# Kernel optimization log

Hardware: AMD Instinct MI355X
Metric: run time of the kernel (lower is better)

Reference implementation:

```python
import jax, jax.numpy as jnp
import numpy as np

N = 16384
C = 4        # in_channels
K = 16       # neighbors
H = 64       # mlp width


def setup_inputs() -> dict:
    key = jax.random.key(0)
    k0, k1, k2, k3, k4 = jax.random.split(key, 5)
    x = jax.random.normal(k0, (N, C), dtype=jnp.float32)
    # nn.Linear(2C, 64) and nn.Linear(64, 64): weight [out, in], bias [out]
    W1 = jax.random.normal(k1, (H, 2 * C), dtype=jnp.float32) * (1.0 / np.sqrt(2 * C))
    b1 = jax.random.normal(k2, (H,), dtype=jnp.float32) * 0.01
    W2 = jax.random.normal(k3, (H, H), dtype=jnp.float32) * (1.0 / np.sqrt(H))
    b2 = jax.random.normal(k4, (H,), dtype=jnp.float32) * 0.01
    return {"x": x, "W1": W1, "b1": b1, "W2": W2, "b2": b2}


def reference(x, W1, b1, W2, b2):
    # x: [N, C] single point cloud (torch code unsqueezes batch dim 0)
    xs = jax.lax.stop_gradient(x)  # knn indices computed under no_grad
    # pairwise = -||xi - xj||^2 = 2*xi.xj - ||xi||^2 - ||xj||^2
    xx = jnp.sum(xs * xs, axis=1)                      # [N]
    pairwise = 2.0 * (xs @ xs.T) - xx[:, None] - xx[None, :]  # [N, N]
    _, idx = jax.lax.top_k(pairwise, K)                # [N, K] (self included, dist 0 is max)
    neigh = x[idx]                                     # [N, K, C] gather
    center = jnp.broadcast_to(x[:, None, :], (x.shape[0], K, C))
    edge = jnp.concatenate([neigh - center, center], axis=-1)  # [N, K, 2C]
    h = jax.nn.relu(jnp.einsum('nkc,hc->nkh', edge, W1) + b1)
    h = jax.nn.relu(jnp.einsum('nkh,gh->nkg', h, W2) + b2)     # [N, K, H]
    out = jnp.mean(h, axis=1)                          # [N, H]
    return out[None]                                   # [1, N, H] matches torch output
```

## Files before the change

### kernel.cpp

```cpp
#include <hip/hip_runtime.h>
#include <math.h>

#define N_PTS 16384
#define K_NBR 16
#define H_DIM 64
#define CAP   38
#define NBLK  (N_PTS / 16)
#define HBLK  (NBLK / 2)
#define PBLK  (HBLK / 4)

typedef unsigned long long u64;
typedef unsigned short u16;
typedef float v2f   __attribute__((ext_vector_type(2)));
typedef float f32x4 __attribute__((ext_vector_type(4)));
typedef short bf16x8 __attribute__((ext_vector_type(8)));

__device__ __forceinline__ u64 mkkey(unsigned vbits, unsigned idx) {
    unsigned of = vbits ^ (unsigned)(((int)vbits >> 31) | 0x80000000);
    return ((u64)of << 32) | (unsigned)(~idx);
}
__device__ __forceinline__ unsigned keyidx(u64 k) { return ~(unsigned)k; }

__device__ __forceinline__ float readlane_f(float v, int l) {
    return __uint_as_float(__builtin_amdgcn_readlane(__float_as_uint(v), l));
}

__device__ __forceinline__ unsigned ofsbits(float f) {
    unsigned b = __float_as_uint(f);
    return b ^ ((unsigned)((int)b >> 31) | 0x80000000u);
}
__device__ __forceinline__ float inv_ofs(unsigned u) {
    return __uint_as_float(u ^ (~(unsigned)((int)u >> 31) | 0x80000000u));
}

__device__ __forceinline__ u16 f2bf(float f) {
    unsigned u = __float_as_uint(f);
    return (u16)((u + 0x7FFFu + ((u >> 16) & 1u)) >> 16);
}
__device__ __forceinline__ float bf2f(u16 b) {
    return __uint_as_float(((unsigned)b) << 16);
}

__device__ __forceinline__ float wave_sort_f32(float v, int lane) {
#pragma unroll
    for (int k = 2; k <= 64; k <<= 1) {
#pragma unroll
        for (int j = k >> 1; j > 0; j >>= 1) {
            float o = __shfl_xor(v, j, 64);
            bool keep_min = (((lane & k) == 0) == ((lane & j) == 0));
            v = keep_min ? fminf(v, o) : fmaxf(v, o);
        }
    }
    return v;
}
__device__ __forceinline__ u64 wave_sort_u64(u64 v, int lane) {
#pragma unroll
    for (int k = 2; k <= 64; k <<= 1) {
#pragma unroll
        for (int j = k >> 1; j > 0; j >>= 1) {
            u64 o = __shfl_xor((unsigned long long)v, j, 64);
            bool keep_min = (((lane & k) == 0) == ((lane & j) == 0));
            u64 mn = (v < o) ? v : o;
            u64 mx = (v < o) ? o : v;
            v = keep_min ? mn : mx;
        }
    }
    return v;
}
__device__ __forceinline__ u64 half32_sort_u64(u64 v, int lane) {
    const int l = lane & 31;
#pragma unroll
    for (int k = 2; k <= 32; k <<= 1) {
#pragma unroll
        for (int j = k >> 1; j > 0; j >>= 1) {
            u64 o = __shfl_xor((unsigned long long)v, j, 64);
            bool keep_min = (((l & k) == 0) == ((l & j) == 0));
            u64 mn = (v < o) ? v : o;
            u64 mx = (v < o) ? o : v;
            v = keep_min ? mn : mx;
        }
    }
    return v;
}

struct CompRes { int nc; float tau; };
__device__ __attribute__((noinline)) CompRes wave_compact(uint2* buf, int cnt,
                                                          int lane) {
    float lm = -INFINITY;
    for (int s = lane; s < cnt; s += 64)
        lm = fmaxf(lm, __uint_as_float(buf[s].x));
    const float tv = readlane_f(wave_sort_f32(lm, lane), 48);
    int nc = 0;
    for (int s0 = 0; s0 < cnt; s0 += 64) {
        const int s = s0 + lane;
        uint2 e = make_uint2(0u, 0u);
        bool keep = false;
        if (s < cnt) { e = buf[s]; keep = (__uint_as_float(e.x) >= tv); }
        const u64 km = __ballot(keep);
        if (keep) {
            int pfx = (int)__popcll(km & ((1ull << lane) - 1));
            buf[nc + pfx] = e;
        }
        nc += (int)__popcll(km);
    }
    CompRes r; r.nc = nc; r.tau = tv;
    return r;
}

__global__ __launch_bounds__(256) void prep_kernel(const float4* __restrict__ x4,
                                                   u16* __restrict__ bf) {
    const int i = blockIdx.x * 256 + threadIdx.x;
    const float4 v = x4[i];
    float xx;
    {
#pragma clang fp contract(off)
        float s0 = v.x * v.x, s1 = v.y * v.y, s2 = v.z * v.z, s3 = v.w * v.w;
        xx = ((s0 + s1) + s2) + s3;
    }
    float c[4] = {v.x, v.y, v.z, v.w};
    u16 H[4], M[4], L[4];
#pragma unroll
    for (int q = 0; q < 4; ++q) {
        float f = c[q];
        u16 h = f2bf(f);            float fh = bf2f(h);
        u16 m = f2bf(f - fh);       float fm = bf2f(m);
        u16 l = f2bf(f - fh - fm);
        H[q] = h; M[q] = m; L[q] = l;
    }
    const float nx = -xx;
    u16 X0 = f2bf(nx);              float x0f = bf2f(X0);
    u16 X1 = f2bf(nx - x0f);        float x1f = bf2f(X1);
    u16 X2 = f2bf(nx - x0f - x1f);
    u16 o[32];
#pragma unroll
    for (int q = 0; q < 4; ++q) {
        o[q]      = H[q];
        o[4 + q]  = M[q];
        o[8 + q]  = H[q];
        o[12 + q] = L[q];
        o[16 + q] = H[q];
        o[20 + q] = M[q];
    }
    o[24] = X0; o[25] = X1; o[26] = X2;
    o[27] = 0; o[28] = 0; o[29] = 0; o[30] = 0; o[31] = 0;
    uint4* dst = (uint4*)(bf + (size_t)i * 32);
#pragma unroll
    for (int q2 = 0; q2 < 4; ++q2) {
        uint4 w;
        w.x = (unsigned)o[q2 * 8 + 0] | ((unsigned)o[q2 * 8 + 1] << 16);
        w.y = (unsigned)o[q2 * 8 + 2] | ((unsigned)o[q2 * 8 + 3] << 16);
        w.z = (unsigned)o[q2 * 8 + 4] | ((unsigned)o[q2 * 8 + 5] << 16);
        w.w = (unsigned)o[q2 * 8 + 6] | ((unsigned)o[q2 * 8 + 7] << 16);
        dst[q2] = w;
    }
}

__global__ __launch_bounds__(256, 4) void knn_kernel(
        const float4* __restrict__ x4,
        const u16* __restrict__ bfrag,
        unsigned* __restrict__ vals,
        u16* __restrict__ idxs) {
    __shared__ __align__(16) uint2 buf[4][16][CAP];
    __shared__ unsigned tau_sh[16];
    const int lane = threadIdx.x & 63;
    const int wave = threadIdx.x >> 6;
    const int q    = lane & 15;
    const int g    = lane >> 4;
    const int qgrp = blockIdx.x >> 1;
    const int half = blockIdx.x & 1;
    const int rowbase = qgrp * 16;
    const int pblk = half * HBLK + wave * PBLK;

    const float4 xi = x4[rowbase + q];
    u16 Ha[4], Ma[4], La[4];
    {
        float yy[4] = {2.f * xi.x, 2.f * xi.y, 2.f * xi.z, 2.f * xi.w};
#pragma unroll
        for (int c = 0; c < 4; ++c) {
            u16 h = f2bf(yy[c]);             float fh = bf2f(h);
            u16 m = f2bf(yy[c] - fh);        float fm = bf2f(m);
            u16 l = f2bf(yy[c] - fh - fm);
            Ha[c] = h; Ma[c] = m; La[c] = l;
        }
    }
    bf16x8 qfrag;
    {
        const u16 ONEB = 0x3F80;
#pragma unroll
        for (int c = 0; c < 4; ++c) {
            u16 lo, hi;
            if (g == 0)      { lo = Ha[c]; hi = Ha[c]; }
            else if (g == 1) { lo = Ma[c]; hi = Ha[c]; }
            else if (g == 2) { lo = La[c]; hi = Ma[c]; }
            else             { lo = (c < 3) ? ONEB : 0; hi = 0; }
            qfrag[c]     = (short)lo;
            qfrag[c + 4] = (short)hi;
        }
    }
    const f32x4 zacc = {0.f, 0.f, 0.f, 0.f};
    const bf16x8* bp = (const bf16x8*)bfrag + (size_t)pblk * 64 + (q * 4 + g);

    f32x4 mx = {-INFINITY, -INFINITY, -INFINITY, -INFINITY};
    {
        bf16x8 A0[4], A1[4];
#pragma unroll
        for (int i = 0; i < 4; ++i) A0[i] = bp[(2 * i) * 64];
#pragma unroll
        for (int i = 0; i < 4; ++i) A1[i] = bp[(8 + 2 * i) * 64];
        const bf16x8* pa = bp + 16 * 64;

#define PROCA(BUF) do {                                                      \
    _Pragma("unroll")                                                        \
    for (int i = 0; i < 4; ++i) {                                            \
        const f32x4 aa = __builtin_amdgcn_mfma_f32_16x16x32_bf16(            \
            BUF[i], qfrag, zacc, 0, 0, 0);                                   \
        mx[0] = fmaxf(mx[0], aa[0]); mx[1] = fmaxf(mx[1], aa[1]);            \
        mx[2] = fmaxf(mx[2], aa[2]); mx[3] = fmaxf(mx[3], aa[3]);            \
    }                                                                        \
} while (0)

        for (int it = 0; it < 7; ++it) {
            PROCA(A0);
#pragma unroll
            for (int i = 0; i < 4; ++i) A0[i] = pa[(2 * i) * 64];
            PROCA(A1);
#pragma unroll
            for (int i = 0; i < 4; ++i) A1[i] = pa[(8 + 2 * i) * 64];
            pa += 16 * 64;
        }
        PROCA(A0);
        PROCA(A1);
#undef PROCA
    }

    {
        float* am = (float*)&buf[0][0][0];
        const int base = wave * 256 + q * 16 + g * 4;
        am[base + 0] = mx[0]; am[base + 1] = mx[1];
        am[base + 2] = mx[2]; am[base + 3] = mx[3];
        __syncthreads();
#pragma unroll
        for (int rr = 0; rr < 4; ++rr) {
            const int r = wave * 4 + rr;
            float v = am[(lane >> 4) * 256 + r * 16 + (lane & 15)];
            v = wave_sort_f32(v, lane);
            if (lane == 48) tau_sh[r] = ofsbits(v);
        }
        __syncthreads();
    }
    float tau = inv_ofs(tau_sh[q]);

    unsigned cq = 0;
    uint2* bq = &buf[wave][q][0];
    const unsigned gid4 = (unsigned)(g * 4);

#define INSERT4(AV, CB) do {                                                 \
    for (;;) {                                                               \
        const bool k0 = (AV)[0] >= tau, k1 = (AV)[1] >= tau;                 \
        const bool k2 = (AV)[2] >= tau, k3 = (AV)[3] >= tau;                 \
        const int cnt = (int)k0 + (int)k1 + (int)k2 + (int)k3;               \
        const int sa = __shfl_xor(cnt, 16, 64);                              \
        const int sb = __shfl_xor(cnt, 32, 64);                              \
        const int sc = __shfl_xor(sa, 32, 64);                               \
        const int tot = cnt + sa + sb + sc;                                  \
        const int pf  = ((g & 1) ? sa : 0) + ((g & 2) ? (sb + sc) : 0);      \
        const u64 ovm = __ballot(cq + (unsigned)tot > CAP);                  \
        if (__builtin_expect(ovm == 0, 1)) {                                 \
            unsigned slot = cq + (unsigned)pf;                               \
            if (k0) bq[slot++] = make_uint2(__float_as_uint((AV)[0]), (CB)); \
            if (k1) bq[slot++] = make_uint2(__float_as_uint((AV)[1]), (CB)+1);\
            if (k2) bq[slot++] = make_uint2(__float_as_uint((AV)[2]), (CB)+2);\
            if (k3) bq[slot++] = make_uint2(__float_as_uint((AV)[3]), (CB)+3);\
            cq += (unsigned)tot;                                             \
            break;                                                           \
        }                                                                    \
        u64 ov = ovm & 0xFFFFull;                                            \
        while (ov) {                                                         \
            const int r = (int)__builtin_ctzll(ov); ov &= ov - 1;            \
            const unsigned cr =                                              \
                (unsigned)__builtin_amdgcn_readlane((int)cq, r);             \
            CompRes res = wave_compact(&buf[wave][r][0], (int)cr, lane);     \
            if (q == r) { cq = (unsigned)res.nc;                             \
                          tau = fmaxf(tau, res.tau); }                       \
        }                                                                    \
    }                                                                        \
} while (0)

#define PROC4(BUF, TB) do {                                                  \
    f32x4 A4_[4];                                                            \
    _Pragma("unroll")                                                        \
    for (int i = 0; i < 4; ++i)                                              \
        A4_[i] = __builtin_amdgcn_mfma_f32_16x16x32_bf16(BUF[i], qfrag,      \
                                                         zacc, 0, 0, 0);     \
    _Pragma("unroll")                                                        \
    for (int i = 0; i < 4; ++i) {                                            \
        const f32x4 av = A4_[i];                                             \
        const float m4 = fmaxf(fmaxf(av[0], av[1]), fmaxf(av[2], av[3]));    \
        if (__ballot(m4 >= tau))                                             \
            INSERT4(av, (unsigned)(((TB) + i) * 16) + gid4);                 \
    }                                                                        \
} while (0)

    {
        bf16x8 B0[4], B1[4];
#pragma unroll
        for (int i = 0; i < 4; ++i) B0[i] = bp[i * 64];
#pragma unroll
        for (int i = 0; i < 4; ++i) B1[i] = bp[(4 + i) * 64];
        const bf16x8* pA = bp + 8 * 64;
        const bf16x8* pB = bp + 12 * 64;

        int t = 0;
        for (; t < PBLK - 8; t += 8) {
            PROC4(B0, pblk + t);
#pragma unroll
            for (int i = 0; i < 4; ++i) B0[i] = pA[i * 64];
            pA += 8 * 64;
            PROC4(B1, pblk + t + 4);
#pragma unroll
            for (int i = 0; i < 4; ++i) B1[i] = pB[i * 64];
            pB += 8 * 64;
        }
        PROC4(B0, pblk + t);
        PROC4(B1, pblk + t + 4);
    }
#undef PROC4
#undef INSERT4

#pragma unroll 1
    for (int r = 0; r < 16; ++r) {
        int c = __builtin_amdgcn_readlane((int)cq, r);
        uint2* br = &buf[wave][r][0];
        if (c <= 16) {
            if (lane < 16) {
                u64 key = 0;
                if (lane < c) { const uint2 e = br[lane]; key = mkkey(e.x, e.y); }
                *(u64*)&buf[wave][r][lane] = key;
            }
        } else {
            u64 key = 0;
            if (lane < c) { const uint2 e = br[lane]; key = mkkey(e.x, e.y); }
            key = wave_sort_u64(key, lane);
            if (lane >= 48)
                *(u64*)&buf[wave][r][lane - 48] = key;
        }
    }

    __syncthreads();
#pragma unroll
    for (int rr = 0; rr < 4; ++rr) {
        const int r2 = wave * 4 + rr;
        u64 key = *(const u64*)&buf[lane >> 4][r2][lane & 15];
        key = wave_sort_u64(key, lane);
        if (lane >= 48) {
            const int o = (rowbase + r2) * 32 + half * 16 + (lane - 48);
            vals[o] = (unsigned)(key >> 32);
            idxs[o] = (u16)keyidx(key);
        }
    }
}

__global__ __launch_bounds__(256, 2) void mlp_kernel(
        const float4* __restrict__ x4,
        const unsigned* __restrict__ vals,
        const u16* __restrict__ idxs,
        const float4* __restrict__ W2f4,
        const float* __restrict__ W1,
        const float* __restrict__ b1,
        const float* __restrict__ b2,
        float* __restrict__ out) {
    __shared__ __align__(16) float4 w2s[16][64];
    __shared__ __align__(16) float  h1s[4][32][68];
    __shared__ __align__(16) float4 xjs[4][32];
    const int lane = threadIdx.x & 63;
    const int wave = threadIdx.x >> 6;
    const int kq   = lane >> 4;
    const int gp   = lane & 15;
    const int p0   = (blockIdx.x * 4 + wave) * 2;

    for (int q = threadIdx.x; q < 1024; q += 256)
        w2s[q & 15][q >> 4] = W2f4[q];
    __syncthreads();

    float w1r[8];
#pragma unroll
    for (int c = 0; c < 8; ++c) w1r[c] = W1[lane * 8 + c];
    const float b1r = b1[lane];
    float b2r[4];
#pragma unroll
    for (int gq = 0; gq < 4; ++gq) b2r[gq] = b2[gq * 16 + gp];

    {
        const int pp = lane >> 5;
        const int j  = lane & 31;
        const int o  = (p0 + pp) * 32 + j;
        u64 key = ((u64)vals[o] << 32) | (unsigned)(~(unsigned)idxs[o]);
        key = half32_sort_u64(key, lane);
        if ((lane & 31) >= 16) {
            const int nb = (int)((~(unsigned)key) & 0xFFFFu);
            xjs[wave][pp * 16 + ((lane & 31) - 16)] = x4[nb];
        }
    }

#pragma unroll
    for (int pp = 0; pp < 2; ++pp) {
        const float4 xi = x4[p0 + pp];
        float hb = b1r;
        hb = fmaf(w1r[4] - w1r[0], xi.x, hb);
        hb = fmaf(w1r[5] - w1r[1], xi.y, hb);
        hb = fmaf(w1r[6] - w1r[2], xi.z, hb);
        hb = fmaf(w1r[7] - w1r[3], xi.w, hb);
#pragma unroll
        for (int k = 0; k < K_NBR; ++k) {
            const float4 xj = xjs[wave][pp * 16 + k];
            float h = hb;
            h = fmaf(w1r[0], xj.x, h);
            h = fmaf(w1r[1], xj.y, h);
            h = fmaf(w1r[2], xj.z, h);
            h = fmaf(w1r[3], xj.w, h);
            h1s[wave][pp * 16 + k][lane] = fmaxf(h, 0.0f);
        }
    }

    v2f acc[2][4][4];
#pragma unroll
    for (int pp = 0; pp < 2; ++pp)
#pragma unroll
        for (int kk = 0; kk < 4; ++kk)
#pragma unroll
            for (int gq = 0; gq < 4; ++gq)
                acc[pp][kk][gq] = (v2f){b2r[gq], 0.0f};

#pragma unroll
    for (int h4 = 0; h4 < 16; ++h4) {
        float4 w4[4];
#pragma unroll
        for (int gq = 0; gq < 4; ++gq) w4[gq] = w2s[h4][gq * 16 + gp];
#pragma unroll
        for (int pp = 0; pp < 2; ++pp) {
#pragma unroll
            for (int kk = 0; kk < 4; ++kk) {
                const float4 hv =
                    *(const float4*)&h1s[wave][pp * 16 + kq * 4 + kk][h4 * 4];
#pragma unroll
                for (int gq = 0; gq < 4; ++gq) {
                    acc[pp][kk][gq] = __builtin_elementwise_fma(
                        (v2f){hv.x, hv.y}, (v2f){w4[gq].x, w4[gq].y},
                        acc[pp][kk][gq]);
                    acc[pp][kk][gq] = __builtin_elementwise_fma(
                        (v2f){hv.z, hv.w}, (v2f){w4[gq].z, w4[gq].w},
                        acc[pp][kk][gq]);
                }
            }
        }
    }

#pragma unroll
    for (int pp = 0; pp < 2; ++pp) {
        float s[4];
#pragma unroll
        for (int gq = 0; gq < 4; ++gq) {
            s[gq] = 0.0f;
#pragma unroll
            for (int kk = 0; kk < 4; ++kk) {
                const float v = acc[pp][kk][gq].x + acc[pp][kk][gq].y;
                s[gq] += fmaxf(v, 0.0f);
            }
        }
#pragma unroll
        for (int off = 16; off <= 32; off <<= 1)
#pragma unroll
            for (int gq = 0; gq < 4; ++gq)
                s[gq] += __shfl_xor(s[gq], off, 64);

        out[(p0 + pp) * H_DIM + kq * 16 + gp] = s[kq] * (1.0f / 16.0f);
    }
}

extern "C" void kernel_launch(void* const* d_in, const int* in_sizes, int n_in,
                              void* d_out, int out_size, void* d_ws, size_t ws_size,
                              hipStream_t stream) {
    (void)in_sizes; (void)n_in; (void)out_size; (void)ws_size;
    const float* x  = (const float*)d_in[0];
    const float* W1 = (const float*)d_in[1];
    const float* b1 = (const float*)d_in[2];
    const float* W2 = (const float*)d_in[3];
    const float* b2 = (const float*)d_in[4];
    float* out = (float*)d_out;

    u16*      bfrag = (u16*)d_ws;
    unsigned* vals  = (unsigned*)((char*)d_ws + (1u << 20));
    u16*      idxs  = (u16*)((char*)d_ws + (3u << 20));

    const float4* x4 = (const float4*)x;

    prep_kernel<<<N_PTS / 256, 256, 0, stream>>>(x4, bfrag);
    knn_kernel <<<N_PTS / 16 * 2, 256, 0, stream>>>(x4, bfrag, vals, idxs);
    mlp_kernel <<<N_PTS / 8,   256, 0, stream>>>(
        x4, vals, idxs, (const float4*)W2, W1, b1, b2, out);
}
```

Before: 219.7 us.

## Process 32 queries per KNN block to reuse candidate fragment loads

```diff
diff --git a/kernel.cpp b/kernel.cpp
--- a/kernel.cpp
+++ b/kernel.cpp
@@ -4,6 +4,7 @@
 #define N_PTS 16384
 #define K_NBR 16
 #define H_DIM 64
+#define QPB   32
 #define CAP   38
 #define NBLK  (N_PTS / 16)
 #define HBLK  (NBLK / 2)
@@ -107,6 +108,31 @@
     return r;
 }
 
+__device__ __forceinline__ bf16x8 make_qfrag(float4 xi, int g) {
+    u16 Ha[4], Ma[4], La[4];
+    float yy[4] = {2.f * xi.x, 2.f * xi.y, 2.f * xi.z, 2.f * xi.w};
+#pragma unroll
+    for (int c = 0; c < 4; ++c) {
+        u16 h = f2bf(yy[c]);             float fh = bf2f(h);
+        u16 m = f2bf(yy[c] - fh);        float fm = bf2f(m);
+        u16 l = f2bf(yy[c] - fh - fm);
+        Ha[c] = h; Ma[c] = m; La[c] = l;
+    }
+    const u16 ONEB = 0x3F80;
+    bf16x8 qf;
+#pragma unroll
+    for (int c = 0; c < 4; ++c) {
+        u16 lo, hi;
+        if (g == 0)      { lo = Ha[c]; hi = Ha[c]; }
+        else if (g == 1) { lo = Ma[c]; hi = Ha[c]; }
+        else if (g == 2) { lo = La[c]; hi = Ma[c]; }
+        else             { lo = (c < 3) ? ONEB : 0; hi = 0; }
+        qf[c]     = (short)lo;
+        qf[c + 4] = (short)hi;
+    }
+    return qf;
+}
+
 __global__ __launch_bounds__(256) void prep_kernel(const float4* __restrict__ x4,
                                                    u16* __restrict__ bf) {
     const int i = blockIdx.x * 256 + threadIdx.x;
@@ -160,144 +186,112 @@
         const u16* __restrict__ bfrag,
         unsigned* __restrict__ vals,
         u16* __restrict__ idxs) {
-    __shared__ __align__(16) uint2 buf[4][16][CAP];
-    __shared__ unsigned tau_sh[16];
+    __shared__ __align__(16) uint2 buf[4][QPB][CAP];
+    __shared__ unsigned tau_sh[QPB];
     const int lane = threadIdx.x & 63;
     const int wave = threadIdx.x >> 6;
     const int q    = lane & 15;
     const int g    = lane >> 4;
     const int qgrp = blockIdx.x >> 1;
     const int half = blockIdx.x & 1;
-    const int rowbase = qgrp * 16;
+    const int qbase = qgrp * QPB;
     const int pblk = half * HBLK + wave * PBLK;
 
-    const float4 xi = x4[rowbase + q];
-    u16 Ha[4], Ma[4], La[4];
-    {
-        float yy[4] = {2.f * xi.x, 2.f * xi.y, 2.f * xi.z, 2.f * xi.w};
-#pragma unroll
-        for (int c = 0; c < 4; ++c) {
-            u16 h = f2bf(yy[c]);             float fh = bf2f(h);
-            u16 m = f2bf(yy[c] - fh);        float fm = bf2f(m);
-            u16 l = f2bf(yy[c] - fh - fm);
-            Ha[c] = h; Ma[c] = m; La[c] = l;
-        }
-    }
-    bf16x8 qfrag;
-    {
-        const u16 ONEB = 0x3F80;
-#pragma unroll
-        for (int c = 0; c < 4; ++c) {
-            u16 lo, hi;
-            if (g == 0)      { lo = Ha[c]; hi = Ha[c]; }
-            else if (g == 1) { lo = Ma[c]; hi = Ha[c]; }
-            else if (g == 2) { lo = La[c]; hi = Ma[c]; }
-            else             { lo = (c < 3) ? ONEB : 0; hi = 0; }
-            qfrag[c]     = (short)lo;
-            qfrag[c + 4] = (short)hi;
-        }
-    }
+    const bf16x8 qf0 = make_qfrag(x4[qbase + q], g);
+    const bf16x8 qf1 = make_qfrag(x4[qbase + 16 + q], g);
     const f32x4 zacc = {0.f, 0.f, 0.f, 0.f};
     const bf16x8* bp = (const bf16x8*)bfrag + (size_t)pblk * 64 + (q * 4 + g);
 
-    f32x4 mx = {-INFINITY, -INFINITY, -INFINITY, -INFINITY};
-    {
-        bf16x8 A0[4], A1[4];
-#pragma unroll
-        for (int i = 0; i < 4; ++i) A0[i] = bp[(2 * i) * 64];
-#pragma unroll
-        for (int i = 0; i < 4; ++i) A1[i] = bp[(8 + 2 * i) * 64];
-        const bf16x8* pa = bp + 16 * 64;
-
-#define PROCA(BUF) do {                                                      \
-    _Pragma("unroll")                                                        \
-    for (int i = 0; i < 4; ++i) {                                            \
-        const f32x4 aa = __builtin_amdgcn_mfma_f32_16x16x32_bf16(            \
-            BUF[i], qfrag, zacc, 0, 0, 0);                                   \
-        mx[0] = fmaxf(mx[0], aa[0]); mx[1] = fmaxf(mx[1], aa[1]);            \
-        mx[2] = fmaxf(mx[2], aa[2]); mx[3] = fmaxf(mx[3], aa[3]);            \
-    }                                                                        \
-} while (0)
-
-        for (int it = 0; it < 7; ++it) {
-            PROCA(A0);
-#pragma unroll
-            for (int i = 0; i < 4; ++i) A0[i] = pa[(2 * i) * 64];
-            PROCA(A1);
-#pragma unroll
-            for (int i = 0; i < 4; ++i) A1[i] = pa[(8 + 2 * i) * 64];
-            pa += 16 * 64;
-        }
-        PROCA(A0);
-        PROCA(A1);
-#undef PROCA
+    f32x4 mx0 = {-INFINITY, -INFINITY, -INFINITY, -INFINITY};
+    f32x4 mx1 = mx0;
+    for (int t = 0; t < PBLK; t += 8) {
+        bf16x8 A0[4];
+#pragma unroll
+        for (int i = 0; i < 4; ++i) A0[i] = bp[(t + 2 * i) * 64];
+#pragma unroll
+        for (int i = 0; i < 4; ++i) {
+            const f32x4 a0 = __builtin_amdgcn_mfma_f32_16x16x32_bf16(
+                A0[i], qf0, zacc, 0, 0, 0);
+            mx0[0] = fmaxf(mx0[0], a0[0]); mx0[1] = fmaxf(mx0[1], a0[1]);
+            mx0[2] = fmaxf(mx0[2], a0[2]); mx0[3] = fmaxf(mx0[3], a0[3]);
+            const f32x4 a1 = __builtin_amdgcn_mfma_f32_16x16x32_bf16(
+                A0[i], qf1, zacc, 0, 0, 0);
+            mx1[0] = fmaxf(mx1[0], a1[0]); mx1[1] = fmaxf(mx1[1], a1[1]);
+            mx1[2] = fmaxf(mx1[2], a1[2]); mx1[3] = fmaxf(mx1[3], a1[3]);
+        }
     }
 
     {
         float* am = (float*)&buf[0][0][0];
-        const int base = wave * 256 + q * 16 + g * 4;
-        am[base + 0] = mx[0]; am[base + 1] = mx[1];
-        am[base + 2] = mx[2]; am[base + 3] = mx[3];
+        const int col = wave * 16 + g * 4;
+#pragma unroll
+        for (int j = 0; j < 4; ++j) {
+            am[q * 64 + col + j]        = mx0[j];
+            am[(16 + q) * 64 + col + j] = mx1[j];
+        }
         __syncthreads();
 #pragma unroll
-        for (int rr = 0; rr < 4; ++rr) {
-            const int r = wave * 4 + rr;
-            float v = am[(lane >> 4) * 256 + r * 16 + (lane & 15)];
+        for (int rr = 0; rr < 8; ++rr) {
+            const int r = wave * 8 + rr;
+            float v = am[r * 64 + lane];
             v = wave_sort_f32(v, lane);
             if (lane == 48) tau_sh[r] = ofsbits(v);
         }
         __syncthreads();
     }
-    float tau = inv_ofs(tau_sh[q]);
-
-    unsigned cq = 0;
-    uint2* bq = &buf[wave][q][0];
+    float tau0 = inv_ofs(tau_sh[q]);
+    float tau1 = inv_ofs(tau_sh[16 + q]);
+
+    unsigned cq0 = 0, cq1 = 0;
+    uint2* bq0 = &buf[wave][q][0];
+    uint2* bq1 = &buf[wave][16 + q][0];
     const unsigned gid4 = (unsigned)(g * 4);
 
-#define INSERT4(AV, CB) do {                                                 \
+#define INSERT4(AV, CB, TAU, CQ, BQ, ROWOFF) do {                            \
     for (;;) {                                                               \
-        const bool k0 = (AV)[0] >= tau, k1 = (AV)[1] >= tau;                 \
-        const bool k2 = (AV)[2] >= tau, k3 = (AV)[3] >= tau;                 \
+        const bool k0 = (AV)[0] >= (TAU), k1 = (AV)[1] >= (TAU);             \
+        const bool k2 = (AV)[2] >= (TAU), k3 = (AV)[3] >= (TAU);             \
         const int cnt = (int)k0 + (int)k1 + (int)k2 + (int)k3;               \
         const int sa = __shfl_xor(cnt, 16, 64);                              \
         const int sb = __shfl_xor(cnt, 32, 64);                              \
         const int sc = __shfl_xor(sa, 32, 64);                               \
         const int tot = cnt + sa + sb + sc;                                  \
         const int pf  = ((g & 1) ? sa : 0) + ((g & 2) ? (sb + sc) : 0);      \
-        const u64 ovm = __ballot(cq + (unsigned)tot > CAP);                  \
+        const u64 ovm = __ballot((CQ) + (unsigned)tot > CAP);                \
         if (__builtin_expect(ovm == 0, 1)) {                                 \
-            unsigned slot = cq + (unsigned)pf;                               \
-            if (k0) bq[slot++] = make_uint2(__float_as_uint((AV)[0]), (CB)); \
-            if (k1) bq[slot++] = make_uint2(__float_as_uint((AV)[1]), (CB)+1);\
-            if (k2) bq[slot++] = make_uint2(__float_as_uint((AV)[2]), (CB)+2);\
-            if (k3) bq[slot++] = make_uint2(__float_as_uint((AV)[3]), (CB)+3);\
-            cq += (unsigned)tot;                                             \
+            unsigned slot = (CQ) + (unsigned)pf;                             \
+            if (k0) (BQ)[slot++] = make_uint2(__float_as_uint((AV)[0]), (CB)); \
+            if (k1) (BQ)[slot++] = make_uint2(__float_as_uint((AV)[1]), (CB)+1);\
+            if (k2) (BQ)[slot++] = make_uint2(__float_as_uint((AV)[2]), (CB)+2);\
+            if (k3) (BQ)[slot++] = make_uint2(__float_as_uint((AV)[3]), (CB)+3);\
+            (CQ) += (unsigned)tot;                                           \
             break;                                                           \
         }                                                                    \
         u64 ov = ovm & 0xFFFFull;                                            \
         while (ov) {                                                         \
             const int r = (int)__builtin_ctzll(ov); ov &= ov - 1;            \
             const unsigned cr =                                              \
-                (unsigned)__builtin_amdgcn_readlane((int)cq, r);             \
-            CompRes res = wave_compact(&buf[wave][r][0], (int)cr, lane);     \
-            if (q == r) { cq = (unsigned)res.nc;                             \
-                          tau = fmaxf(tau, res.tau); }                       \
+                (unsigned)__builtin_amdgcn_readlane((int)(CQ), r);           \
+            CompRes res = wave_compact(&buf[wave][(ROWOFF) + r][0], (int)cr, \
+                                       lane);                                \
+            if (q == r) { (CQ) = (unsigned)res.nc;                           \
+                          (TAU) = fmaxf((TAU), res.tau); }                   \
         }                                                                    \
     }                                                                        \
 } while (0)
 
 #define PROC4(BUF, TB) do {                                                  \
-    f32x4 A4_[4];                                                            \
-    _Pragma("unroll")                                                        \
-    for (int i = 0; i < 4; ++i)                                              \
-        A4_[i] = __builtin_amdgcn_mfma_f32_16x16x32_bf16(BUF[i], qfrag,      \
-                                                         zacc, 0, 0, 0);     \
     _Pragma("unroll")                                                        \
     for (int i = 0; i < 4; ++i) {                                            \
-        const f32x4 av = A4_[i];                                             \
-        const float m4 = fmaxf(fmaxf(av[0], av[1]), fmaxf(av[2], av[3]));    \
-        if (__ballot(m4 >= tau))                                             \
-            INSERT4(av, (unsigned)(((TB) + i) * 16) + gid4);                 \
+        const f32x4 a0 = __builtin_amdgcn_mfma_f32_16x16x32_bf16(            \
+            BUF[i], qf0, zacc, 0, 0, 0);                                     \
+        const f32x4 a1 = __builtin_amdgcn_mfma_f32_16x16x32_bf16(            \
+            BUF[i], qf1, zacc, 0, 0, 0);                                     \
+        const unsigned cb = (unsigned)(((TB) + i) * 16) + gid4;              \
+        const float m0 = fmaxf(fmaxf(a0[0], a0[1]), fmaxf(a0[2], a0[3]));    \
+        if (__ballot(m0 >= tau0)) INSERT4(a0, cb, tau0, cq0, bq0, 0);        \
+        const float m1 = fmaxf(fmaxf(a1[0], a1[1]), fmaxf(a1[2], a1[3]));    \
+        if (__ballot(m1 >= tau1)) INSERT4(a1, cb, tau1, cq1, bq1, 16);       \
     }                                                                        \
 } while (0)
 
@@ -328,8 +322,8 @@
 #undef INSERT4
 
 #pragma unroll 1
-    for (int r = 0; r < 16; ++r) {
-        int c = __builtin_amdgcn_readlane((int)cq, r);
+    for (int r = 0; r < QPB; ++r) {
+        int c = __builtin_amdgcn_readlane((int)((r < 16) ? cq0 : cq1), r & 15);
         uint2* br = &buf[wave][r][0];
         if (c <= 16) {
             if (lane < 16) {
@@ -348,12 +342,12 @@
 
     __syncthreads();
 #pragma unroll
-    for (int rr = 0; rr < 4; ++rr) {
-        const int r2 = wave * 4 + rr;
+    for (int rr = 0; rr < 8; ++rr) {
+        const int r2 = wave * 8 + rr;
         u64 key = *(const u64*)&buf[lane >> 4][r2][lane & 15];
         key = wave_sort_u64(key, lane);
         if (lane >= 48) {
-            const int o = (rowbase + r2) * 32 + half * 16 + (lane - 48);
+            const int o = (qbase + r2) * 32 + half * 16 + (lane - 48);
             vals[o] = (unsigned)(key >> 32);
             idxs[o] = (u16)keyidx(key);
         }
@@ -495,7 +489,7 @@
     const float4* x4 = (const float4*)x;
 
     prep_kernel<<<N_PTS / 256, 256, 0, stream>>>(x4, bfrag);
-    knn_kernel <<<N_PTS / 16 * 2, 256, 0, stream>>>(x4, bfrag, vals, idxs);
+    knn_kernel <<<N_PTS / QPB * 2, 256, 0, stream>>>(x4, bfrag, vals, idxs);
     mlp_kernel <<<N_PTS / 8,   256, 0, stream>>>(
         x4, vals, idxs, (const float4*)W2, W1, b1, b2, out);
 }
```

Result: faster. 204.7 us (median of 2 runs) (-6.8%).

## Replace shared candidate buffer compaction with per-lane top-16 segments in kNN

Applied to the files above, without the earlier changes.

```diff
diff --git a/kernel.cpp b/kernel.cpp
--- a/kernel.cpp
+++ b/kernel.cpp
@@ -4,7 +4,8 @@
 #define N_PTS 16384
 #define K_NBR 16
 #define H_DIM 64
-#define CAP   38
+#define SEGW  17
+#define ROWW  (4 * SEGW)
 #define NBLK  (N_PTS / 16)
 #define HBLK  (NBLK / 2)
 #define PBLK  (HBLK / 4)
@@ -20,10 +21,6 @@
     return ((u64)of << 32) | (unsigned)(~idx);
 }
 __device__ __forceinline__ unsigned keyidx(u64 k) { return ~(unsigned)k; }
-
-__device__ __forceinline__ float readlane_f(float v, int l) {
-    return __uint_as_float(__builtin_amdgcn_readlane(__float_as_uint(v), l));
-}
 
 __device__ __forceinline__ unsigned ofsbits(float f) {
     unsigned b = __float_as_uint(f);
@@ -83,28 +80,29 @@
     return v;
 }
 
-struct CompRes { int nc; float tau; };
-__device__ __attribute__((noinline)) CompRes wave_compact(uint2* buf, int cnt,
-                                                          int lane) {
-    float lm = -INFINITY;
-    for (int s = lane; s < cnt; s += 64)
-        lm = fmaxf(lm, __uint_as_float(buf[s].x));
-    const float tv = readlane_f(wave_sort_f32(lm, lane), 48);
-    int nc = 0;
-    for (int s0 = 0; s0 < cnt; s0 += 64) {
-        const int s = s0 + lane;
-        uint2 e = make_uint2(0u, 0u);
-        bool keep = false;
-        if (s < cnt) { e = buf[s]; keep = (__uint_as_float(e.x) >= tv); }
-        const u64 km = __ballot(keep);
-        if (keep) {
-            int pfx = (int)__popcll(km & ((1ull << lane) - 1));
-            buf[nc + pfx] = e;
-        }
-        nc += (int)__popcll(km);
-    }
-    CompRes r; r.nc = nc; r.tau = tv;
-    return r;
+__device__ __forceinline__ bf16x8 make_qfrag(float4 xi, int g) {
+    u16 Ha[4], Ma[4], La[4];
+    float yy[4] = {2.f * xi.x, 2.f * xi.y, 2.f * xi.z, 2.f * xi.w};
+#pragma unroll
+    for (int c = 0; c < 4; ++c) {
+        u16 h = f2bf(yy[c]);             float fh = bf2f(h);
+        u16 m = f2bf(yy[c] - fh);        float fm = bf2f(m);
+        u16 l = f2bf(yy[c] - fh - fm);
+        Ha[c] = h; Ma[c] = m; La[c] = l;
+    }
+    const u16 ONEB = 0x3F80;
+    bf16x8 qf;
+#pragma unroll
+    for (int c = 0; c < 4; ++c) {
+        u16 lo, hi;
+        if (g == 0)      { lo = Ha[c]; hi = Ha[c]; }
+        else if (g == 1) { lo = Ma[c]; hi = Ha[c]; }
+        else if (g == 2) { lo = La[c]; hi = Ma[c]; }
+        else             { lo = (c < 3) ? ONEB : 0; hi = 0; }
+        qf[c]     = (short)lo;
+        qf[c + 4] = (short)hi;
+    }
+    return qf;
 }
 
 __global__ __launch_bounds__(256) void prep_kernel(const float4* __restrict__ x4,
@@ -160,7 +158,7 @@
         const u16* __restrict__ bfrag,
         unsigned* __restrict__ vals,
         u16* __restrict__ idxs) {
-    __shared__ __align__(16) uint2 buf[4][16][CAP];
+    __shared__ __align__(16) u64 arr[4][16][ROWW];
     __shared__ unsigned tau_sh[16];
     const int lane = threadIdx.x & 63;
     const int wave = threadIdx.x >> 6;
@@ -171,117 +169,66 @@
     const int rowbase = qgrp * 16;
     const int pblk = half * HBLK + wave * PBLK;
 
-    const float4 xi = x4[rowbase + q];
-    u16 Ha[4], Ma[4], La[4];
-    {
-        float yy[4] = {2.f * xi.x, 2.f * xi.y, 2.f * xi.z, 2.f * xi.w};
-#pragma unroll
-        for (int c = 0; c < 4; ++c) {
-            u16 h = f2bf(yy[c]);             float fh = bf2f(h);
-            u16 m = f2bf(yy[c] - fh);        float fm = bf2f(m);
-            u16 l = f2bf(yy[c] - fh - fm);
-            Ha[c] = h; Ma[c] = m; La[c] = l;
-        }
-    }
-    bf16x8 qfrag;
-    {
-        const u16 ONEB = 0x3F80;
-#pragma unroll
-        for (int c = 0; c < 4; ++c) {
-            u16 lo, hi;
-            if (g == 0)      { lo = Ha[c]; hi = Ha[c]; }
-            else if (g == 1) { lo = Ma[c]; hi = Ha[c]; }
-            else if (g == 2) { lo = La[c]; hi = Ma[c]; }
-            else             { lo = (c < 3) ? ONEB : 0; hi = 0; }
-            qfrag[c]     = (short)lo;
-            qfrag[c + 4] = (short)hi;
-        }
-    }
+    const bf16x8 qfrag = make_qfrag(x4[rowbase + q], g);
     const f32x4 zacc = {0.f, 0.f, 0.f, 0.f};
     const bf16x8* bp = (const bf16x8*)bfrag + (size_t)pblk * 64 + (q * 4 + g);
 
     f32x4 mx = {-INFINITY, -INFINITY, -INFINITY, -INFINITY};
+    for (int t = 0; t < PBLK; t += 8) {
+        bf16x8 A0[4];
+#pragma unroll
+        for (int i = 0; i < 4; ++i) A0[i] = bp[(t + 2 * i) * 64];
+#pragma unroll
+        for (int i = 0; i < 4; ++i) {
+            const f32x4 aa = __builtin_amdgcn_mfma_f32_16x16x32_bf16(
+                A0[i], qfrag, zacc, 0, 0, 0);
+            mx[0] = fmaxf(mx[0], aa[0]); mx[1] = fmaxf(mx[1], aa[1]);
+            mx[2] = fmaxf(mx[2], aa[2]); mx[3] = fmaxf(mx[3], aa[3]);
+        }
+    }
+
     {
-        bf16x8 A0[4], A1[4];
-#pragma unroll
-        for (int i = 0; i < 4; ++i) A0[i] = bp[(2 * i) * 64];
-#pragma unroll
-        for (int i = 0; i < 4; ++i) A1[i] = bp[(8 + 2 * i) * 64];
-        const bf16x8* pa = bp + 16 * 64;
-
-#define PROCA(BUF) do {                                                      \
-    _Pragma("unroll")                                                        \
-    for (int i = 0; i < 4; ++i) {                                            \
-        const f32x4 aa = __builtin_amdgcn_mfma_f32_16x16x32_bf16(            \
-            BUF[i], qfrag, zacc, 0, 0, 0);                                   \
-        mx[0] = fmaxf(mx[0], aa[0]); mx[1] = fmaxf(mx[1], aa[1]);            \
-        mx[2] = fmaxf(mx[2], aa[2]); mx[3] = fmaxf(mx[3], aa[3]);            \
-    }                                                                        \
-} while (0)
-
-        for (int it = 0; it < 7; ++it) {
-            PROCA(A0);
-#pragma unroll
-            for (int i = 0; i < 4; ++i) A0[i] = pa[(2 * i) * 64];
-            PROCA(A1);
-#pragma unroll
-            for (int i = 0; i < 4; ++i) A1[i] = pa[(8 + 2 * i) * 64];
-            pa += 16 * 64;
-        }
-        PROCA(A0);
-        PROCA(A1);
-#undef PROCA
-    }
-
-    {
-        float* am = (float*)&buf[0][0][0];
-        const int base = wave * 256 + q * 16 + g * 4;
-        am[base + 0] = mx[0]; am[base + 1] = mx[1];
-        am[base + 2] = mx[2]; am[base + 3] = mx[3];
+        float* am = (float*)&arr[0][0][0];
+        const int col = wave * 16 + g * 4;
+#pragma unroll
+        for (int j = 0; j < 4; ++j) am[q * 64 + col + j] = mx[j];
         __syncthreads();
 #pragma unroll
         for (int rr = 0; rr < 4; ++rr) {
             const int r = wave * 4 + rr;
-            float v = am[(lane >> 4) * 256 + r * 16 + (lane & 15)];
+            float v = am[r * 64 + lane];
             v = wave_sort_f32(v, lane);
             if (lane == 48) tau_sh[r] = ofsbits(v);
         }
         __syncthreads();
     }
-    float tau = inv_ofs(tau_sh[q]);
-
-    unsigned cq = 0;
-    uint2* bq = &buf[wave][q][0];
+    const float tau = inv_ofs(tau_sh[q]);
+
+    {
+        u64* w0 = &arr[wave][0][0];
+        for (int j = lane; j < 16 * ROWW; j += 64) w0[j] = 0;
+    }
+
+    u64* seg = &arr[wave][q][g * SEGW];
+    unsigned myc = 0;
     const unsigned gid4 = (unsigned)(g * 4);
 
-#define INSERT4(AV, CB) do {                                                 \
-    for (;;) {                                                               \
-        const bool k0 = (AV)[0] >= tau, k1 = (AV)[1] >= tau;                 \
-        const bool k2 = (AV)[2] >= tau, k3 = (AV)[3] >= tau;                 \
-        const int cnt = (int)k0 + (int)k1 + (int)k2 + (int)k3;               \
-        const int sa = __shfl_xor(cnt, 16, 64);                              \
-        const int sb = __shfl_xor(cnt, 32, 64);                              \
-        const int sc = __shfl_xor(sa, 32, 64);                               \
-        const int tot = cnt + sa + sb + sc;                                  \
-        const int pf  = ((g & 1) ? sa : 0) + ((g & 2) ? (sb + sc) : 0);      \
-        const u64 ovm = __ballot(cq + (unsigned)tot > CAP);                  \
-        if (__builtin_expect(ovm == 0, 1)) {                                 \
-            unsigned slot = cq + (unsigned)pf;                               \
-            if (k0) bq[slot++] = make_uint2(__float_as_uint((AV)[0]), (CB)); \
-            if (k1) bq[slot++] = make_uint2(__float_as_uint((AV)[1]), (CB)+1);\
-            if (k2) bq[slot++] = make_uint2(__float_as_uint((AV)[2]), (CB)+2);\
-            if (k3) bq[slot++] = make_uint2(__float_as_uint((AV)[3]), (CB)+3);\
-            cq += (unsigned)tot;                                             \
-            break;                                                           \
-        }                                                                    \
-        u64 ov = ovm & 0xFFFFull;                                            \
-        while (ov) {                                                         \
-            const int r = (int)__builtin_ctzll(ov); ov &= ov - 1;            \
-            const unsigned cr =                                              \
-                (unsigned)__builtin_amdgcn_readlane((int)cq, r);             \
-            CompRes res = wave_compact(&buf[wave][r][0], (int)cr, lane);     \
-            if (q == r) { cq = (unsigned)res.nc;                             \
-                          tau = fmaxf(tau, res.tau); }                       \
+#define INSERT(AV, CB) do {                                                  \
+    _Pragma("unroll")                                                        \
+    for (int r_ = 0; r_ < 4; ++r_) {                                         \
+        if ((AV)[r_] >= tau) {                                               \
+            const u64 key_ = mkkey(__float_as_uint((AV)[r_]), (CB) + r_);    \
+            if (__builtin_expect(myc < 16u, 1)) {                            \
+                seg[myc++] = key_;                                           \
+            } else {                                                         \
+                int mi_ = 0; u64 mv_ = seg[0];                               \
+                _Pragma("unroll")                                            \
+                for (int s_ = 1; s_ < 16; ++s_) {                            \
+                    const u64 v_ = seg[s_];                                  \
+                    if (v_ < mv_) { mv_ = v_; mi_ = s_; }                    \
+                }                                                            \
+                if (key_ > mv_) seg[mi_] = key_;                             \
+            }                                                                \
         }                                                                    \
     }                                                                        \
 } while (0)
@@ -297,7 +244,7 @@
         const f32x4 av = A4_[i];                                             \
         const float m4 = fmaxf(fmaxf(av[0], av[1]), fmaxf(av[2], av[3]));    \
         if (__ballot(m4 >= tau))                                             \
-            INSERT4(av, (unsigned)(((TB) + i) * 16) + gid4);                 \
+            INSERT(av, (unsigned)(((TB) + i) * 16) + gid4);                  \
     }                                                                        \
 } while (0)
 
@@ -325,32 +272,21 @@
         PROC4(B1, pblk + t + 4);
     }
 #undef PROC4
-#undef INSERT4
+#undef INSERT
 
 #pragma unroll 1
     for (int r = 0; r < 16; ++r) {
-        int c = __builtin_amdgcn_readlane((int)cq, r);
-        uint2* br = &buf[wave][r][0];
-        if (c <= 16) {
-            if (lane < 16) {
-                u64 key = 0;
-                if (lane < c) { const uint2 e = br[lane]; key = mkkey(e.x, e.y); }
-                *(u64*)&buf[wave][r][lane] = key;
-            }
-        } else {
-            u64 key = 0;
-            if (lane < c) { const uint2 e = br[lane]; key = mkkey(e.x, e.y); }
-            key = wave_sort_u64(key, lane);
-            if (lane >= 48)
-                *(u64*)&buf[wave][r][lane - 48] = key;
-        }
+        u64 key = arr[wave][r][(lane >> 4) * SEGW + (lane & 15)];
+        key = wave_sort_u64(key, lane);
+        if (lane >= 48)
+            arr[wave][r][lane - 48] = key;
     }
 
     __syncthreads();
 #pragma unroll
     for (int rr = 0; rr < 4; ++rr) {
         const int r2 = wave * 4 + rr;
-        u64 key = *(const u64*)&buf[lane >> 4][r2][lane & 15];
+        u64 key = arr[lane >> 4][r2][lane & 15];
         key = wave_sort_u64(key, lane);
         if (lane >= 48) {
             const int o = (rowbase + r2) * 32 + half * 16 + (lane - 48);
```

Result: slower. 254.5 us (+15.9%).
